# Kernel tuning notes

Hardware: AMD Instinct MI355X
Metric: run time of the kernel (lower is better)

The kernel has to match this reference:

```python
import jax, jax.numpy as jnp
import numpy as np

FWD_W = 1.0
BWD_W = 1.0
EPS = 1e-12  # guard sqrt gradient at exact zero


def setup_inputs() -> dict:
    key = jax.random.key(0)
    k1, k2 = jax.random.split(key)
    pred = jax.random.normal(k1, (4, 8192, 3), dtype=jnp.float32)
    target = jax.random.normal(k2, (4, 8192, 3), dtype=jnp.float32)
    return {"pred": pred, "target": target}


def reference(pred, target):
    # pairwise Euclidean distances (torch.cdist, p=2): (B, N, M)
    sq = (jnp.sum(pred * pred, axis=-1)[:, :, None]
          + jnp.sum(target * target, axis=-1)[:, None, :]
          - 2.0 * jnp.einsum('bnd,bmd->bnm', pred, target))
    dist = jnp.sqrt(jnp.maximum(sq, EPS))
    forward_dist = jnp.min(dist, axis=2)   # (B, N): pred -> nearest target
    backward_dist = jnp.min(dist, axis=1)  # (B, M): target -> nearest pred
    total = FWD_W * jnp.sum(forward_dist, axis=1) + BWD_W * jnp.sum(backward_dist, axis=1)
    return jnp.mean(total)  # reduction='mean'
```

## Files before the change

kernel.cpp:

```cpp
#include <hip/hip_runtime.h>
#include <math.h>

#define BATCH   4
#define NPTS    8192
#define THREADS 256
#define NQTOT   (2 * BATCH * NPTS)
#define CHUNK   1024
#define TSPLIT  4
#define THALF   (NPTS / TSPLIT)
#define NCHUNKS (THALF / CHUNK)

typedef _Float16 h8  __attribute__((ext_vector_type(8)));
typedef float    f16v __attribute__((ext_vector_type(16)));

__device__ __forceinline__ void glds16(const void* g, void* l)
{
    __builtin_amdgcn_global_load_lds(
        (const __attribute__((address_space(1))) unsigned int*)g,
        (__attribute__((address_space(3))) unsigned int*)l, 16, 0, 0);
}

__global__ __launch_bounds__(THREADS)
void chamfer_transform(const float* __restrict__ pred,
                       const float* __restrict__ target,
                       h8* __restrict__ trans_lo,
                       h8* __restrict__ trans_hi)
{
    const int p   = blockIdx.x * THREADS + threadIdx.x;
    const int arr = p >> 15;
    const int pb  = p & 32767;

    const float* src = (arr ? target : pred) + (size_t)pb * 3;
    const float x = src[0], y = src[1], z = src[2];

    const _Float16 hx = (_Float16)x;  const float lxf = x - (float)hx;
    const _Float16 hy = (_Float16)y;  const float lyf = y - (float)hy;
    const _Float16 hz = (_Float16)z;  const float lzf = z - (float)hz;
    const _Float16 lx = (_Float16)lxf, ly = (_Float16)lyf, lz = (_Float16)lzf;

    const float tx = (float)hx + (float)lx;
    const float ty = (float)hy + (float)ly;
    const float tz = (float)hz + (float)lz;
    const float tt = fmaf(tx, tx, fmaf(ty, ty, tz * tz));
    const _Float16 tth = (_Float16)tt;
    const _Float16 ttl = (_Float16)(tt - (float)tth);

    const _Float16 n2 = (_Float16)(-2.0f);
    h8 lo = { n2 * hx, n2 * hy, n2 * hz, tth,
              n2 * hx, n2 * hy, n2 * hz, ttl };
    h8 hi = { n2 * lx, n2 * ly, n2 * lz, (_Float16)0.0f,
              (_Float16)0.0f, (_Float16)0.0f, (_Float16)0.0f, (_Float16)0.0f };

    trans_lo[p] = lo;
    trans_hi[p] = hi;
}

__device__ __forceinline__ h8 make_afrag(const float* __restrict__ qp, const int hi)
{
    const float x = qp[0], y = qp[1], z = qp[2];
    const _Float16 hx = (_Float16)x; const _Float16 lx = (_Float16)(x - (float)hx);
    const _Float16 hy = (_Float16)y; const _Float16 ly = (_Float16)(y - (float)hy);
    const _Float16 hz = (_Float16)z; const _Float16 lz = (_Float16)(z - (float)hz);
    const _Float16 one  = (_Float16)1.0f;
    const _Float16 zero = (_Float16)0.0f;
    if (hi == 0) return (h8){hx, hy, hz, one, lx, ly, lz, one};
    return (h8){hx, hy, hz, zero, zero, zero, zero, zero};
}

__global__ __launch_bounds__(THREADS, 4)
void chamfer_min_kernel(const float* __restrict__ pred,
                        const float* __restrict__ target,
                        const h8* __restrict__ trans_lo,
                        const h8* __restrict__ trans_hi,
                        float* __restrict__ partial)
{
    __shared__ uint4 slo[CHUNK];
    __shared__ uint4 shi[CHUNK];

    const int tid  = threadIdx.x;
    const int lane = tid & 63;
    const int wave = tid >> 6;
    const int n    = lane & 31;
    const int hi   = lane >> 5;

    const int bid = blockIdx.x;
    const int ts  = bid & 3;
    const int qg  = (bid >> 2) & 31;
    const int b   = (bid >> 7) & 3;
    const int dir = bid >> 9;

    const int  qtbase = qg * 256 + wave * 64;
    const int  tbase  = ts * THALF;
    const int  darr   = dir ^ 1;
    const float* qraw = ((dir == 0) ? pred : target) + (size_t)b * NPTS * 3;

    const h8 afrag0 = make_afrag(qraw + (size_t)(qtbase + n) * 3, hi);
    const h8 afrag1 = make_afrag(qraw + (size_t)(qtbase + 32 + n) * 3, hi);

    float mn0[16], mn1[16];
    #pragma unroll
    for (int i = 0; i < 16; ++i) { mn0[i] = 3.0e38f; mn1[i] = 3.0e38f; }

    const size_t gbase = (size_t)(darr * 4 + b) * NPTS + tbase;
    const h8* bsrc = hi ? (const h8*)shi : (const h8*)slo;
    const f16v zc = {};

    for (int c = 0; c < NCHUNKS; ++c) {
        const size_t cb = gbase + (size_t)c * CHUNK;
        #pragma unroll
        for (int r = 0; r < 4; ++r) {
            glds16(((const uint4*)trans_lo) + cb + r * THREADS + tid,
                   &slo[r * THREADS + tid]);
            glds16(((const uint4*)trans_hi) + cb + r * THREADS + tid,
                   &shi[r * THREADS + tid]);
        }
        __syncthreads();

        for (int tp = 0; tp < CHUNK / 64; ++tp) {
            const h8 b0 = bsrc[tp * 64 + n];
            const h8 b1 = bsrc[tp * 64 + 32 + n];

            const f16v d00 = __builtin_amdgcn_mfma_f32_32x32x16_f16(afrag0, b0, zc, 0, 0, 0);
            const f16v d01 = __builtin_amdgcn_mfma_f32_32x32x16_f16(afrag0, b1, zc, 0, 0, 0);
            #pragma unroll
            for (int i = 0; i < 16; ++i)
                mn0[i] = fminf(fminf(d00[i], d01[i]), mn0[i]);

            const f16v d10 = __builtin_amdgcn_mfma_f32_32x32x16_f16(afrag1, b0, zc, 0, 0, 0);
            const f16v d11 = __builtin_amdgcn_mfma_f32_32x32x16_f16(afrag1, b1, zc, 0, 0, 0);
            #pragma unroll
            for (int i = 0; i < 16; ++i)
                mn1[i] = fminf(fminf(d10[i], d11[i]), mn1[i]);
        }
        __syncthreads();
    }

    #pragma unroll
    for (int mask = 1; mask <= 16; mask <<= 1) {
        #pragma unroll
        for (int i = 0; i < 16; ++i) {
            mn0[i] = fminf(mn0[i], __shfl_xor(mn0[i], mask, 64));
            mn1[i] = fminf(mn1[i], __shfl_xor(mn1[i], mask, 64));
        }
    }

    if (n == 0) {
        float* dst = partial + (size_t)ts * NQTOT
                   + (size_t)(dir * 4 + b) * NPTS + qtbase;
        #pragma unroll
        for (int i = 0; i < 16; ++i) {
            const int row = (i & 3) + 8 * (i >> 2) + 4 * hi;
            dst[row]      = mn0[i];
            dst[32 + row] = mn1[i];
        }
    }
}

__global__ __launch_bounds__(THREADS)
void chamfer_reduce1(const float* __restrict__ partial,
                     const float* __restrict__ pred,
                     const float* __restrict__ target,
                     float* __restrict__ bsum)
{
    const int tid = threadIdx.x;
    const int i   = blockIdx.x * THREADS + tid;

    const float m01 = fminf(partial[i],                 partial[NQTOT + i]);
    const float m23 = fminf(partial[2 * NQTOT + i],     partial[3 * NQTOT + i]);
    const float m   = fminf(m01, m23);

    const int dir  = i >> 15;
    const int rest = i & 32767;
    const float* qp = ((dir == 0) ? pred : target) + (size_t)rest * 3;
    const float x = qp[0], y = qp[1], z = qp[2];
    const float qq = fmaf(x, x, fmaf(y, y, z * z));

    float acc = sqrtf(fmaxf(qq + m, 1e-12f));

    #pragma unroll
    for (int off = 32; off > 0; off >>= 1)
        acc += __shfl_down(acc, off, 64);

    __shared__ float wsum[4];
    if ((tid & 63) == 0) wsum[tid >> 6] = acc;
    __syncthreads();
    if (tid == 0) bsum[blockIdx.x] = wsum[0] + wsum[1] + wsum[2] + wsum[3];
}

__global__ __launch_bounds__(THREADS)
void chamfer_reduce2(const float* __restrict__ bsum,
                     float* __restrict__ out)
{
    const int tid = threadIdx.x;
    float v = bsum[tid];
    #pragma unroll
    for (int off = 32; off > 0; off >>= 1)
        v += __shfl_down(v, off, 64);

    __shared__ float wsum[4];
    if ((tid & 63) == 0) wsum[tid >> 6] = v;
    __syncthreads();
    if (tid == 0) out[0] = (wsum[0] + wsum[1] + wsum[2] + wsum[3]) * (1.0f / BATCH);
}

extern "C" void kernel_launch(void* const* d_in, const int* in_sizes, int n_in,
                              void* d_out, int out_size, void* d_ws, size_t ws_size,
                              hipStream_t stream)
{
    const float* pred   = (const float*)d_in[0];
    const float* target = (const float*)d_in[1];
    float* out          = (float*)d_out;

    h8*    trans_lo = (h8*)d_ws;
    h8*    trans_hi = (h8*)((char*)d_ws + (size_t)65536 * 16);
    float* partial  = (float*)((char*)d_ws + (size_t)131072 * 16);
    float* bsum     = partial + (size_t)TSPLIT * NQTOT;

    chamfer_transform<<<NQTOT / THREADS, THREADS, 0, stream>>>(
        pred, target, trans_lo, trans_hi);

    chamfer_min_kernel<<<2 * BATCH * 32 * TSPLIT, THREADS, 0, stream>>>(
        pred, target, trans_lo, trans_hi, partial);

    chamfer_reduce1<<<NQTOT / THREADS, THREADS, 0, stream>>>(
        partial, pred, target, bsum);

    chamfer_reduce2<<<1, THREADS, 0, stream>>>(bsum, out);
}
```

Baseline: 85.55 us.

## Interleave lo/hi fragments and load B operands directly from global memory

The transform kernel now writes the lo and hi fp16 fragments interleaved in a single buffer. The min kernel drops the LDS staging and its __syncthreads, and each lane reads its B fragment straight from global memory (through the cache), with the loop unrolled by two. This removes barrier stalls and LDS traffic. In exchange, every wave in a block reloads the same target data from L1/L2 and must rely on the cache to hide latency.

```diff
diff --git a/kernel.cpp b/kernel.cpp
--- a/kernel.cpp
+++ b/kernel.cpp
@@ -5,26 +5,16 @@
 #define NPTS    8192
 #define THREADS 256
 #define NQTOT   (2 * BATCH * NPTS)
-#define CHUNK   1024
 #define TSPLIT  4
 #define THALF   (NPTS / TSPLIT)
-#define NCHUNKS (THALF / CHUNK)
 
 typedef _Float16 h8  __attribute__((ext_vector_type(8)));
 typedef float    f16v __attribute__((ext_vector_type(16)));
-
-__device__ __forceinline__ void glds16(const void* g, void* l)
-{
-    __builtin_amdgcn_global_load_lds(
-        (const __attribute__((address_space(1))) unsigned int*)g,
-        (__attribute__((address_space(3))) unsigned int*)l, 16, 0, 0);
-}
 
 __global__ __launch_bounds__(THREADS)
 void chamfer_transform(const float* __restrict__ pred,
                        const float* __restrict__ target,
-                       h8* __restrict__ trans_lo,
-                       h8* __restrict__ trans_hi)
+                       h8* __restrict__ trans_il)
 {
     const int p   = blockIdx.x * THREADS + threadIdx.x;
     const int arr = p >> 15;
@@ -51,8 +41,8 @@
     h8 hi = { n2 * lx, n2 * ly, n2 * lz, (_Float16)0.0f,
               (_Float16)0.0f, (_Float16)0.0f, (_Float16)0.0f, (_Float16)0.0f };
 
-    trans_lo[p] = lo;
-    trans_hi[p] = hi;
+    trans_il[2 * p]     = lo;
+    trans_il[2 * p + 1] = hi;
 }
 
 __device__ __forceinline__ h8 make_afrag(const float* __restrict__ qp, const int hi)
@@ -70,13 +60,9 @@
 __global__ __launch_bounds__(THREADS, 4)
 void chamfer_min_kernel(const float* __restrict__ pred,
                         const float* __restrict__ target,
-                        const h8* __restrict__ trans_lo,
-                        const h8* __restrict__ trans_hi,
+                        const h8* __restrict__ trans_il,
                         float* __restrict__ partial)
 {
-    __shared__ uint4 slo[CHUNK];
-    __shared__ uint4 shi[CHUNK];
-
     const int tid  = threadIdx.x;
     const int lane = tid & 63;
     const int wave = tid >> 6;
@@ -102,37 +88,25 @@
     for (int i = 0; i < 16; ++i) { mn0[i] = 3.0e38f; mn1[i] = 3.0e38f; }
 
     const size_t gbase = (size_t)(darr * 4 + b) * NPTS + tbase;
-    const h8* bsrc = hi ? (const h8*)shi : (const h8*)slo;
+    const h8* bp = trans_il + 2 * (gbase + n) + hi;
     const f16v zc = {};
 
-    for (int c = 0; c < NCHUNKS; ++c) {
-        const size_t cb = gbase + (size_t)c * CHUNK;
-        #pragma unroll
-        for (int r = 0; r < 4; ++r) {
-            glds16(((const uint4*)trans_lo) + cb + r * THREADS + tid,
-                   &slo[r * THREADS + tid]);
-            glds16(((const uint4*)trans_hi) + cb + r * THREADS + tid,
-                   &shi[r * THREADS + tid]);
-        }
-        __syncthreads();
-
-        for (int tp = 0; tp < CHUNK / 64; ++tp) {
-            const h8 b0 = bsrc[tp * 64 + n];
-            const h8 b1 = bsrc[tp * 64 + 32 + n];
-
-            const f16v d00 = __builtin_amdgcn_mfma_f32_32x32x16_f16(afrag0, b0, zc, 0, 0, 0);
-            const f16v d01 = __builtin_amdgcn_mfma_f32_32x32x16_f16(afrag0, b1, zc, 0, 0, 0);
-            #pragma unroll
-            for (int i = 0; i < 16; ++i)
-                mn0[i] = fminf(fminf(d00[i], d01[i]), mn0[i]);
-
-            const f16v d10 = __builtin_amdgcn_mfma_f32_32x32x16_f16(afrag1, b0, zc, 0, 0, 0);
-            const f16v d11 = __builtin_amdgcn_mfma_f32_32x32x16_f16(afrag1, b1, zc, 0, 0, 0);
-            #pragma unroll
-            for (int i = 0; i < 16; ++i)
-                mn1[i] = fminf(fminf(d10[i], d11[i]), mn1[i]);
-        }
-        __syncthreads();
+    #pragma unroll 2
+    for (int tp = 0; tp < THALF / 64; ++tp) {
+        const h8 b0 = bp[tp * 128];
+        const h8 b1 = bp[tp * 128 + 64];
+
+        const f16v d00 = __builtin_amdgcn_mfma_f32_32x32x16_f16(afrag0, b0, zc, 0, 0, 0);
+        const f16v d01 = __builtin_amdgcn_mfma_f32_32x32x16_f16(afrag0, b1, zc, 0, 0, 0);
+        #pragma unroll
+        for (int i = 0; i < 16; ++i)
+            mn0[i] = fminf(fminf(d00[i], d01[i]), mn0[i]);
+
+        const f16v d10 = __builtin_amdgcn_mfma_f32_32x32x16_f16(afrag1, b0, zc, 0, 0, 0);
+        const f16v d11 = __builtin_amdgcn_mfma_f32_32x32x16_f16(afrag1, b1, zc, 0, 0, 0);
+        #pragma unroll
+        for (int i = 0; i < 16; ++i)
+            mn1[i] = fminf(fminf(d10[i], d11[i]), mn1[i]);
     }
 
     #pragma unroll
@@ -211,16 +185,15 @@
     const float* target = (const float*)d_in[1];
     float* out          = (float*)d_out;
 
-    h8*    trans_lo = (h8*)d_ws;
-    h8*    trans_hi = (h8*)((char*)d_ws + (size_t)65536 * 16);
+    h8*    trans_il = (h8*)d_ws;
     float* partial  = (float*)((char*)d_ws + (size_t)131072 * 16);
     float* bsum     = partial + (size_t)TSPLIT * NQTOT;
 
     chamfer_transform<<<NQTOT / THREADS, THREADS, 0, stream>>>(
-        pred, target, trans_lo, trans_hi);
+        pred, target, trans_il);
 
     chamfer_min_kernel<<<2 * BATCH * 32 * TSPLIT, THREADS, 0, stream>>>(
-        pred, target, trans_lo, trans_hi, partial);
+        pred, target, trans_il, partial);
 
     chamfer_reduce1<<<NQTOT / THREADS, THREADS, 0, stream>>>(
         partial, pred, target, bsum);
```

New measurement: 83.45 us. -2.5%, faster.
